# Kernel optimization log

Measured on AMD Instinct MI355X. Metric: run time of the kernel, lower is better.

The kernel has to match this reference:

```python
import jax, jax.numpy as jnp
import numpy as np

N = 65536      # samples
DX = 1024      # X features
DY = 1024      # Y features
D = 256        # projected width (x_net/y_net output)
LAMX = 0.1
LAMY = 0.1
SIGMA = 0.5    # STG gate noise std (eval-mode deterministic gate)
EPS = 0.001    # regularizer used in original code


def setup_inputs() -> dict:
    key = jax.random.key(0)
    ks = jax.random.split(key, 8)
    X = jax.random.normal(ks[0], (N, DX), dtype=jnp.float32)
    Y = jax.random.normal(ks[1], (N, DY), dtype=jnp.float32)
    # StochasticGates params (mu per input feature)
    mu_x = 0.01 * jax.random.normal(ks[2], (DX,), dtype=jnp.float32)
    mu_y = 0.01 * jax.random.normal(ks[3], (DY,), dtype=jnp.float32)
    # per-view linear nets (x_net: DX->D, y_net: DY->D)
    Wx = jax.random.normal(ks[4], (DX, D), dtype=jnp.float32) / np.sqrt(DX)
    bx = jnp.zeros((D,), dtype=jnp.float32)
    Wy = jax.random.normal(ks[5], (DY, D), dtype=jnp.float32) / np.sqrt(DY)
    by = jnp.zeros((D,), dtype=jnp.float32)
    return {"X": X, "Y": Y, "mu_x": mu_x, "mu_y": mu_y,
            "Wx": Wx, "bx": bx, "Wy": Wy, "by": by}


def _stg_gate(mu):
    # deterministic (eval) hard gate: clamp(mu + 0.5, 0, 1)
    return jnp.clip(mu + 0.5, 0.0, 1.0)


def _stg_reg(mu, lam):
    # lam * mean(P(gate > 0)) = lam * mean(Phi(mu/sigma))  [Gaussian CDF]
    return lam * jnp.mean(0.5 * (1.0 + jax.lax.erf(mu / (SIGMA * jnp.sqrt(2.0)))))


def _cov(a, b):
    # matches torch: (b.T @ a).T / (N-1) == a.T @ b / (N-1)
    n = a.shape[0]
    return (a.T @ b) / (n - 1)


def _inv_sqrt_sym(A):
    # A^(-1/2) via eigendecomposition; A symmetric so eigh == eig with V^-1 = V.T
    w, V = jnp.linalg.eigh(A)
    return (V * (w + EPS) ** (-0.5)) @ V.T


def _corr(Xh, Yh):
    d = Xh.shape[1]
    psi_x = Xh - Xh.mean(axis=0)
    psi_y = Yh - Yh.mean(axis=0)
    C_yy = _cov(psi_y, psi_y)
    C_yx = _cov(psi_y, psi_x)
    C_xy = _cov(psi_x, psi_y)
    C_xx = _cov(psi_x, psi_x)
    I = jnp.eye(d, dtype=Xh.dtype)
    C_yy_inv_root = _inv_sqrt_sym(C_yy + EPS * I)
    C_xx_inv = jnp.linalg.inv(C_xx + EPS * I)
    M = C_yy_inv_root @ C_yx @ C_xx_inv @ C_xy @ C_yy_inv_root
    return jnp.trace(M) / d


def reference(X, Y, mu_x, mu_y, Wx, bx, Wy, by):
    Xh = (X * _stg_gate(mu_x)) @ Wx + bx   # [N, D]
    Yh = (Y * _stg_gate(mu_y)) @ Wy + by   # [N, D]
    loss = -_corr(Xh, Yh) + _stg_reg(mu_x, LAMX) + _stg_reg(mu_y, LAMY)
    return loss
```

## Files before the change

kernel.cpp:

```cpp
#include <hip/hip_runtime.h>

#define N_S   65536
#define DXF   1024
#define DD    256
#define NM1   65535.0f
#define EPSR  0.001f

typedef __attribute__((ext_vector_type(4)))  float          f32x4;
typedef __attribute__((ext_vector_type(16))) float          f32x16;
typedef __attribute__((ext_vector_type(8)))  short          bf16x8;
typedef __attribute__((ext_vector_type(4)))  unsigned short ushort4_t;
typedef __attribute__((ext_vector_type(8)))  unsigned short ushort8_t;

__device__ __forceinline__ unsigned short f2bf(float f){
  unsigned u = __float_as_uint(f);
  u += 0x7fffu + ((u >> 16) & 1u);
  return (unsigned short)(u >> 16);
}
__device__ __forceinline__ float bf2f(unsigned short h){
  return __uint_as_float(((unsigned)h) << 16);
}
__device__ __forceinline__ f32x4 mfma16(bf16x8 a, bf16x8 b, f32x4 c){
  return __builtin_amdgcn_mfma_f32_16x16x32_bf16(a, b, c, 0, 0, 0);
}
__device__ __forceinline__ f32x16 mfma32(bf16x8 a, bf16x8 b, f32x16 c){
  return __builtin_amdgcn_mfma_f32_32x32x16_bf16(a, b, c, 0, 0, 0);
}
__device__ __forceinline__ void gld_lds16(const void* g, void* l){
  __builtin_amdgcn_global_load_lds(
      (const __attribute__((address_space(1))) unsigned int*)g,
      (__attribute__((address_space(3))) unsigned int*)l, 16, 0, 0);
}
__device__ __forceinline__ bf16x8 pack8(float4 a, float4 b){
  union { unsigned u[4]; bf16x8 v; } r;
  asm("v_cvt_pk_bf16_f32 %0, %1, %2" : "=v"(r.u[0]) : "v"(a.x), "v"(a.y));
  asm("v_cvt_pk_bf16_f32 %0, %1, %2" : "=v"(r.u[1]) : "v"(a.z), "v"(a.w));
  asm("v_cvt_pk_bf16_f32 %0, %1, %2" : "=v"(r.u[2]) : "v"(b.x), "v"(b.y));
  asm("v_cvt_pk_bf16_f32 %0, %1, %2" : "=v"(r.u[3]) : "v"(b.z), "v"(b.w));
  return r.v;
}

__global__ void k_prep(const float* __restrict__ Wx, const float* __restrict__ Wy,
                       const float* __restrict__ mux, const float* __restrict__ muy,
                       unsigned short* __restrict__ WTx, unsigned short* __restrict__ WTy,
                       float* __restrict__ scal){
  int v = blockIdx.y;
  const float* W  = v ? Wy  : Wx;
  const float* mu = v ? muy : mux;
  unsigned short* WT = v ? WTy : WTx;
  int j = threadIdx.x;
  if (j < 4){
    float ph = 0.5f * (1.f + erff(mu[blockIdx.x * 4 + j] * 1.41421356237f));
    atomicAdd(scal + 2 + v, 9.765625e-5f * ph);
  }
  #pragma unroll
  for (int r = 0; r < 4; ++r){
    int k = blockIdx.x * 4 + r;
    float g = fminf(fmaxf(mu[k] + 0.5f, 0.f), 1.f);
    WT[(size_t)(k >> 3) * 2048 + j * 8 + (k & 7)] = f2bf(g * W[(size_t)k * DD + j]);
  }
}

__global__ __launch_bounds__(256, 4) void k_gemm5(
    const float* __restrict__ X, const float* __restrict__ Y,
    const unsigned short* __restrict__ WTx, const unsigned short* __restrict__ WTy,
    unsigned short* __restrict__ Xhb, unsigned short* __restrict__ Yhb){
  const float* A = blockIdx.z ? Y : X;
  const unsigned short* WT = blockIdx.z ? WTy : WTx;
  unsigned short* Out = blockIdx.z ? Yhb : Xhb;

  __shared__ unsigned short As[64][40];
  __shared__ unsigned short Bs[2][4][256][8];

  int tid = threadIdx.x, lane = tid & 63, wid = tid >> 6;
  int wr = wid >> 1, wc = wid & 1;
  int row0 = blockIdx.x * 64;

  f32x4 acc[2][8] = {};

  int s_row = tid >> 2, s_kq = tid & 3;
  const float* ap = A + (size_t)(row0 + s_row) * DXF + s_kq * 8;

  auto stageB = [&](int buf, int ks){
    #pragma unroll
    for (int i = 0; i < 4; ++i)
      gld_lds16(WT + (size_t)(ks * 4 + i) * 2048 + (wid * 64 + lane) * 8,
                &Bs[buf][i][wid * 64][0]);
  };

  float4 a0, a1, n0, n1;
  stageB(0, 0);
  asm volatile("" ::: "memory");
  a0 = *(const float4*)(ap);
  a1 = *(const float4*)(ap + 4);

  for (int ks = 0; ks < 32; ++ks){
    asm volatile("s_waitcnt vmcnt(2)" ::: "memory");
    __builtin_amdgcn_s_barrier();
    if (ks + 1 < 32){
      stageB((ks + 1) & 1, ks + 1);
      asm volatile("" ::: "memory");
      n0 = *(const float4*)(ap + (ks + 1) * 32);
      n1 = *(const float4*)(ap + (ks + 1) * 32 + 4);
      asm volatile("s_waitcnt vmcnt(6)" ::: "memory");
    } else {
      asm volatile("s_waitcnt vmcnt(0)" ::: "memory");
    }
    *(bf16x8*)&As[s_row][s_kq * 8] = pack8(a0, a1);
    asm volatile("s_waitcnt lgkmcnt(0)" ::: "memory");
    __builtin_amdgcn_s_barrier();

    int bb = ks & 1;
    bf16x8 af0 = *(const bf16x8*)&As[wr * 32 + (lane & 15)][(lane >> 4) * 8];
    bf16x8 af1 = *(const bf16x8*)&As[wr * 32 + 16 + (lane & 15)][(lane >> 4) * 8];
    #pragma unroll
    for (int ni = 0; ni < 8; ++ni){
      bf16x8 bf = *(const bf16x8*)&Bs[bb][lane >> 4][wc * 128 + ni * 16 + (lane & 15)][0];
      acc[0][ni] = mfma16(af0, bf, acc[0][ni]);
      acc[1][ni] = mfma16(af1, bf, acc[1][ni]);
    }
    a0 = n0; a1 = n1;
  }

  __syncthreads();
  unsigned short* tl = &Bs[0][0][0][0];
  #pragma unroll
  for (int p = 0; p < 2; ++p){
    if (wr == p){
      #pragma unroll
      for (int mi = 0; mi < 2; ++mi)
        #pragma unroll
        for (int ni = 0; ni < 8; ++ni)
          #pragma unroll
          for (int rr = 0; rr < 4; ++rr){
            int r = mi * 16 + (lane >> 4) * 4 + rr;
            int c = wc * 128 + ni * 16 + (lane & 15);
            tl[r * 256 + c] = f2bf(acc[mi][ni][rr]);
          }
    }
    __syncthreads();
    unsigned short* ob = Out + (size_t)(row0 + p * 32) * DD;
    #pragma unroll
    for (int r = 0; r < 4; ++r){
      int off = r * 2048 + tid * 8;
      *(ushort8_t*)(ob + off) = *(const ushort8_t*)(tl + off);
    }
    if (p == 0) __syncthreads();
  }
}

__global__ __launch_bounds__(512) void k_gram(
    const unsigned short* __restrict__ Xhb, const unsigned short* __restrict__ Yhb,
    float* __restrict__ part, float* __restrict__ sx, float* __restrict__ sy, int P){
  int type = blockIdx.z;
  int p = blockIdx.x;
  int chunk = N_S / P;
  int r0 = p * chunk;
  const unsigned short* Asrc = (type == 0) ? Xhb : Yhb;
  const unsigned short* Bsrc = (type == 1) ? Yhb : Xhb;
  bool dualB = (type == 2);

  __shared__ unsigned short At[256][40];
  __shared__ unsigned short Bt[256][40];

  int tid = threadIdx.x;
  int lane = tid & 63, wid = tid >> 6;
  int wr = wid >> 1, wc = wid & 1;

  f32x4 acc[4][8] = {};
  float cs0 = 0.f, cs1 = 0.f;

  int cp  = tid & 127;
  int kb0 = tid >> 7;

  unsigned ua[2][4], ub[2][4];

  auto loadT = [&](int ks){
    int base = r0 + ks * 32;
    #pragma unroll
    for (int r = 0; r < 2; ++r){
      int kb = kb0 + r * 4;
      #pragma unroll
      for (int kr = 0; kr < 4; ++kr){
        ua[r][kr] = *(const unsigned*)(Asrc + (size_t)(base + kb * 4 + kr) * DD + cp * 2);
        if (dualB)
          ub[r][kr] = *(const unsigned*)(Bsrc + (size_t)(base + kb * 4 + kr) * DD + cp * 2);
      }
    }
  };
  auto storeT = [&](){
    #pragma unroll
    for (int r = 0; r < 2; ++r){
      int kb = kb0 + r * 4;
      ushort4_t lo = { (unsigned short)ua[r][0], (unsigned short)ua[r][1],
                       (unsigned short)ua[r][2], (unsigned short)ua[r][3] };
      ushort4_t hi = { (unsigned short)(ua[r][0] >> 16), (unsigned short)(ua[r][1] >> 16),
                       (unsigned short)(ua[r][2] >> 16), (unsigned short)(ua[r][3] >> 16) };
      *(ushort4_t*)&At[cp * 2][kb * 4]     = lo;
      *(ushort4_t*)&At[cp * 2 + 1][kb * 4] = hi;
      if (type < 2){
        #pragma unroll
        for (int kr = 0; kr < 4; ++kr){
          cs0 += bf2f((unsigned short)ua[r][kr]);
          cs1 += bf2f((unsigned short)(ua[r][kr] >> 16));
        }
      }
      if (dualB){
        ushort4_t lob = { (unsigned short)ub[r][0], (unsigned short)ub[r][1],
                          (unsigned short)ub[r][2], (unsigned short)ub[r][3] };
        ushort4_t hib = { (unsigned short)(ub[r][0] >> 16), (unsigned short)(ub[r][1] >> 16),
                          (unsigned short)(ub[r][2] >> 16), (unsigned short)(ub[r][3] >> 16) };
        *(ushort4_t*)&Bt[cp * 2][kb * 4]     = lob;
        *(ushort4_t*)&Bt[cp * 2 + 1][kb * 4] = hib;
      }
    }
  };

  unsigned short (*Btp)[40] = dualB ? Bt : At;

  int KS = chunk / 32;
  loadT(0);
  for (int ks = 0; ks < KS; ++ks){
    __syncthreads();
    storeT();
    __syncthreads();
    if (ks + 1 < KS) loadT(ks + 1);
    bf16x8 af[4], bfv[8];
    #pragma unroll
    for (int mi = 0; mi < 4; ++mi)
      af[mi] = *(const bf16x8*)&At[wr * 64 + mi * 16 + (lane & 15)][(lane >> 4) * 8];
    #pragma unroll
    for (int ni = 0; ni < 8; ++ni)
      bfv[ni] = *(const bf16x8*)&Btp[wc * 128 + ni * 16 + (lane & 15)][(lane >> 4) * 8];
    #pragma unroll
    for (int mi = 0; mi < 4; ++mi)
      #pragma unroll
      for (int ni = 0; ni < 8; ++ni)
        acc[mi][ni] = mfma16(af[mi], bfv[ni], acc[mi][ni]);
  }

  float* dst = part + ((size_t)p * 3 + type) * 65536;
  #pragma unroll
  for (int mi = 0; mi < 4; ++mi)
    #pragma unroll
    for (int ni = 0; ni < 8; ++ni)
      #pragma unroll
      for (int rr = 0; rr < 4; ++rr){
        int grow = wr * 64 + mi * 16 + (lane >> 4) * 4 + rr;
        int gcol = wc * 128 + ni * 16 + (lane & 15);
        dst[(size_t)grow * 256 + gcol] = acc[mi][ni][rr];
      }

  if (type < 2){
    __syncthreads();
    float* red = (float*)&At[0][0];
    red[kb0 * 256 + cp * 2]     = cs0;
    red[kb0 * 256 + cp * 2 + 1] = cs1;
    __syncthreads();
    if (tid < 256){
      float s = red[tid] + red[256 + tid] + red[512 + tid] + red[768 + tid];
      atomicAdd((type == 0 ? sx : sy) + tid, s);
    }
  }
}

__global__ void k_reduce(const float* __restrict__ part, const float* __restrict__ sx,
                         const float* __restrict__ sy, float* __restrict__ Am,
                         float* __restrict__ Bm,
                         unsigned short* __restrict__ Abf, unsigned short* __restrict__ Bbf,
                         unsigned short* __restrict__ Cbf, unsigned short* __restrict__ CbfT,
                         float* __restrict__ scal, int P){
  __shared__ float r2[256];
  int i = blockIdx.x, j = threadIdx.x;
  size_t idx = (size_t)i * 256 + j;
  float gxx = 0.f, gyy = 0.f, gyx = 0.f;
  for (int p = 0; p < P; ++p){
    const float* b = part + (size_t)p * 3 * 65536;
    gxx += b[idx];
    gyy += b[65536 + idx];
    gyx += b[131072 + idx];
  }
  float invn1 = 1.f / NM1;
  float invn  = 1.f / (float)N_S;
  float sxi = sx[i], sxj = sx[j], syi = sy[i], syj = sy[j];
  float diag = (i == j) ? 1.f : 0.f;
  float am = (gyy - syi * syj * invn) * invn1 + diag * (2.f * EPSR);
  float bm = (gxx - sxi * sxj * invn) * invn1 + diag * EPSR;
  float cv = (gyx - syi * sxj * invn) * invn1;
  Am[idx] = am;  Bm[idx] = bm;
  Abf[idx] = f2bf(am);
  Bbf[idx] = f2bf(bm);
  Cbf[idx] = f2bf(cv);
  CbfT[(size_t)j * 256 + i] = f2bf(cv);
  r2[j] = fabsf(am);
  __syncthreads();
  for (int s = 128; s > 0; s >>= 1){ if (j < s) r2[j] += r2[j + s]; __syncthreads(); }
  if (j == 0) atomicMax((unsigned*)scal + 5, __float_as_uint(r2[0]));
  __syncthreads();
  r2[j] = fabsf(bm);
  __syncthreads();
  for (int s = 128; s > 0; s >>= 1){ if (j < s) r2[j] += r2[j + s]; __syncthreads(); }
  if (j == 0) atomicMax((unsigned*)scal + 6, __float_as_uint(r2[0]));
}

__global__ void k_x1(const float* __restrict__ Am, const float* __restrict__ Bm,
                     unsigned short* __restrict__ X0, const float* __restrict__ scal){
  int m = blockIdx.y;
  const unsigned* su = (const unsigned*)scal;
  float al = 1.9f / __uint_as_float(su[5 + m]);
  const float* M = m ? Bm : Am;
  int e = blockIdx.x * 512 + threadIdx.x;
  float v = -al * al * M[e];
  if ((e >> 8) == (e & 255)) v += 2.f * al;
  X0[m * 65536 + e] = f2bf(v);
}

__global__ __launch_bounds__(512) void k_it(
    const unsigned short* __restrict__ Abf, const unsigned short* __restrict__ Bbf,
    const unsigned short* __restrict__ Xc, unsigned short* __restrict__ Xn){
  int m = blockIdx.y, j = blockIdx.x;
  const unsigned short* M  = m ? Bbf : Abf;
  const unsigned short* Xm = Xc + m * 65536;
  unsigned short*       Xo = Xn + m * 65536;

  __shared__ unsigned short XJ[32 * 256];
  __shared__ unsigned short TT[32 * 256];

  int tid = threadIdx.x, lane = tid & 63, w = tid >> 6;
  int r31 = lane & 31, kh = lane >> 5;

  #pragma unroll
  for (int i = 0; i < 2; ++i){
    int rl = w * 4 + i * 2 + kh;
    int cg = ((lane & 31) - rl) & 31;
    gld_lds16(Xm + (size_t)(j * 32 + rl) * 256 + cg * 8, &XJ[(w * 4 + i * 2) * 256]);
  }
  asm volatile("s_waitcnt vmcnt(0)" ::: "memory");
  __builtin_amdgcn_s_barrier();

  f32x16 acc = {};
  const unsigned short* arow = M + (size_t)(w * 32 + r31) * 256 + kh * 8;
  #pragma unroll
  for (int ks = 0; ks < 16; ++ks){
    bf16x8 af = *(const bf16x8*)(arow + ks * 16);
    int ch = ((ks * 2 + kh) + r31) & 31;
    bf16x8 bf = *(const bf16x8*)&XJ[r31 * 256 + ch * 8];
    acc = mfma32(af, bf, acc);
  }
  #pragma unroll
  for (int reg = 0; reg < 16; ++reg){
    int kk = w * 32 + (reg & 3) + ((reg >> 2) << 3) + (kh << 2);
    int ch = ((kk >> 3) + r31) & 31;
    TT[r31 * 256 + ch * 8 + (kk & 7)] = f2bf(acc[reg]);
  }
  __syncthreads();

  f32x16 acc2 = {};
  const unsigned short* xrow = Xm + (size_t)(w * 32 + r31) * 256 + kh * 8;
  #pragma unroll
  for (int ks = 0; ks < 16; ++ks){
    bf16x8 af = *(const bf16x8*)(xrow + ks * 16);
    int ch = ((ks * 2 + kh) + r31) & 31;
    bf16x8 bf = *(const bf16x8*)&TT[r31 * 256 + ch * 8];
    acc2 = mfma32(af, bf, acc2);
  }
  #pragma unroll
  for (int reg = 0; reg < 16; ++reg){
    int row = w * 32 + (reg & 3) + ((reg >> 2) << 3) + (kh << 2);
    int ch = ((row >> 3) + r31) & 31;
    float xv = bf2f(XJ[r31 * 256 + ch * 8 + (row & 7)]);
    Xo[(size_t)row * 256 + j * 32 + r31] = f2bf(2.f * xv - acc2[reg]);
  }
}

__global__ __launch_bounds__(512) void k_uv(
    const unsigned short* __restrict__ Xf,
    const unsigned short* __restrict__ Cbf, const unsigned short* __restrict__ CbfT,
    float* __restrict__ U, float* __restrict__ W){
  int m = blockIdx.y, j = blockIdx.x;
  __shared__ unsigned short BJ[32 * 256];
  int tid = threadIdx.x, lane = tid & 63, w = tid >> 6;
  int r31 = lane & 31, kh = lane >> 5;
  const unsigned short* Brows = m ? (Xf + 65536) : CbfT;
  const unsigned short* Arows = m ? Cbf : Xf;
  float* D = m ? W : U;

  #pragma unroll
  for (int i = 0; i < 2; ++i){
    int rl = w * 4 + i * 2 + kh;
    int cg = ((lane & 31) - rl) & 31;
    gld_lds16(Brows + (size_t)(j * 32 + rl) * 256 + cg * 8, &BJ[(w * 4 + i * 2) * 256]);
  }
  asm volatile("s_waitcnt vmcnt(0)" ::: "memory");
  __builtin_amdgcn_s_barrier();

  f32x16 acc = {};
  const unsigned short* ar = Arows + (size_t)(w * 32 + r31) * 256 + kh * 8;
  #pragma unroll
  for (int ks = 0; ks < 16; ++ks){
    bf16x8 af = *(const bf16x8*)(ar + ks * 16);
    int ch = ((ks * 2 + kh) + r31) & 31;
    bf16x8 bf = *(const bf16x8*)&BJ[r31 * 256 + ch * 8];
    acc = mfma32(af, bf, acc);
  }
  #pragma unroll
  for (int reg = 0; reg < 16; ++reg){
    int row = w * 32 + (reg & 3) + ((reg >> 2) << 3) + (kh << 2);
    D[(size_t)row * 256 + j * 32 + r31] = acc[reg];
  }
}

__global__ __launch_bounds__(1024) void k_fin(const float* __restrict__ U,
                                              const float* __restrict__ W,
                                              const float* __restrict__ scal,
                                              float* __restrict__ out){
  __shared__ float red[1024];
  int tid = threadIdx.x;
  float t = 0.f;
  #pragma unroll
  for (int r = 0; r < 16; ++r){
    int i = r * 4096 + tid * 4;
    float4 u = *(const float4*)(U + i);
    float4 w = *(const float4*)(W + i);
    t += u.x * w.x + u.y * w.y + u.z * w.z + u.w * w.w;
  }
  red[tid] = t; __syncthreads();
  for (int s = 512; s > 0; s >>= 1){ if (tid < s) red[tid] += red[tid + s]; __syncthreads(); }
  if (tid == 0) out[0] = -red[0] / 256.f + scal[2] + scal[3];
}

extern "C" void kernel_launch(void* const* d_in, const int* in_sizes, int n_in,
                              void* d_out, int out_size, void* d_ws, size_t ws_size,
                              hipStream_t stream){
  (void)in_sizes; (void)n_in; (void)out_size;
  const float* X   = (const float*)d_in[0];
  const float* Y   = (const float*)d_in[1];
  const float* mux = (const float*)d_in[2];
  const float* muy = (const float*)d_in[3];
  const float* Wx  = (const float*)d_in[4];
  const float* Wy  = (const float*)d_in[6];
  float* out = (float*)d_out;
  char* ws = (char*)d_ws;

  const size_t MB = 1ull << 20;
  const size_t KB = 1024;
  size_t oXHB = 0;
  size_t oYHB = 32 * MB;
  size_t oWTX = 64 * MB;
  size_t oWTY = oWTX + 512 * KB;
  size_t oSX  = oWTY + 512 * KB;
  size_t oSY  = oSX + 4 * KB;
  size_t oSC  = oSY + 4 * KB;
  size_t oA   = oSC + 4 * KB;
  size_t oB   = oA   + 256 * KB;
  size_t oABF = oB   + 256 * KB;
  size_t oBBF = oABF + 128 * KB;
  size_t oCBF = oBBF + 128 * KB;
  size_t oCBT = oCBF + 128 * KB;
  size_t oX0  = oCBT + 128 * KB;
  size_t oX1  = oX0  + 256 * KB;
  size_t oTB  = oX1  + 256 * KB;
  size_t oU   = oTB  + 256 * KB;
  size_t oV   = oU   + 256 * KB;
  size_t oPart = 68 * MB;

  size_t per = 3ull * 65536 * 4;
  int P = 128;
  while (P > 8 && oPart + (size_t)P * per > ws_size) P >>= 1;

  unsigned short* Xhb = (unsigned short*)(ws + oXHB);
  unsigned short* Yhb = (unsigned short*)(ws + oYHB);
  unsigned short* WTx = (unsigned short*)(ws + oWTX);
  unsigned short* WTy = (unsigned short*)(ws + oWTY);
  float* sx   = (float*)(ws + oSX);
  float* sy   = (float*)(ws + oSY);
  float* scal = (float*)(ws + oSC);
  float* Am   = (float*)(ws + oA);
  float* Bm   = (float*)(ws + oB);
  unsigned short* Abf  = (unsigned short*)(ws + oABF);
  unsigned short* Bbf  = (unsigned short*)(ws + oBBF);
  unsigned short* Cbf  = (unsigned short*)(ws + oCBF);
  unsigned short* CbfT = (unsigned short*)(ws + oCBT);
  unsigned short* X0   = (unsigned short*)(ws + oX0);
  unsigned short* X1   = (unsigned short*)(ws + oX1);
  float* U    = (float*)(ws + oU);
  float* V    = (float*)(ws + oV);
  float* part = (float*)(ws + oPart);

  hipMemsetAsync(ws + oSX, 0, 12 * KB, stream);

  k_prep<<<dim3(256, 2), 256, 0, stream>>>(Wx, Wy, mux, muy, WTx, WTy, scal);
  k_gemm5<<<dim3(1024, 1, 2), 256, 0, stream>>>(X, Y, WTx, WTy, Xhb, Yhb);
  k_gram<<<dim3(P, 1, 3), 512, 0, stream>>>(Xhb, Yhb, part, sx, sy, P);
  k_reduce<<<256, 256, 0, stream>>>(part, sx, sy, Am, Bm, Abf, Bbf, Cbf, CbfT, scal, P);

  k_x1<<<dim3(128, 2), 512, 0, stream>>>(Am, Bm, X0, scal);
  k_it<<<dim3(8, 2), 512, 0, stream>>>(Abf, Bbf, X0, X1);
  k_it<<<dim3(8, 2), 512, 0, stream>>>(Abf, Bbf, X1, X0);
  k_it<<<dim3(8, 2), 512, 0, stream>>>(Abf, Bbf, X0, X1);
  k_it<<<dim3(8, 2), 512, 0, stream>>>(Abf, Bbf, X1, X0);
  k_it<<<dim3(8, 2), 512, 0, stream>>>(Abf, Bbf, X0, X1);
  k_uv<<<dim3(8, 2), 512, 0, stream>>>(X1, Cbf, CbfT, U, V);
  k_fin<<<1, 1024, 0, stream>>>(U, V, scal, out);
}
```

Baseline: 345.5 us.

## Rework projection GEMM to 512 threads with single-buffered swizzled LDS B tile

```diff
diff --git a/kernel.cpp b/kernel.cpp
--- a/kernel.cpp
+++ b/kernel.cpp
@@ -30,14 +30,6 @@
   __builtin_amdgcn_global_load_lds(
       (const __attribute__((address_space(1))) unsigned int*)g,
       (__attribute__((address_space(3))) unsigned int*)l, 16, 0, 0);
-}
-__device__ __forceinline__ bf16x8 pack8(float4 a, float4 b){
-  union { unsigned u[4]; bf16x8 v; } r;
-  asm("v_cvt_pk_bf16_f32 %0, %1, %2" : "=v"(r.u[0]) : "v"(a.x), "v"(a.y));
-  asm("v_cvt_pk_bf16_f32 %0, %1, %2" : "=v"(r.u[1]) : "v"(a.z), "v"(a.w));
-  asm("v_cvt_pk_bf16_f32 %0, %1, %2" : "=v"(r.u[2]) : "v"(b.x), "v"(b.y));
-  asm("v_cvt_pk_bf16_f32 %0, %1, %2" : "=v"(r.u[3]) : "v"(b.z), "v"(b.w));
-  return r.v;
 }
 
 __global__ void k_prep(const float* __restrict__ Wx, const float* __restrict__ Wy,
@@ -61,7 +53,7 @@
   }
 }
 
-__global__ __launch_bounds__(256, 4) void k_gemm5(
+__global__ __launch_bounds__(512, 8) void k_gemm7(
     const float* __restrict__ X, const float* __restrict__ Y,
     const unsigned short* __restrict__ WTx, const unsigned short* __restrict__ WTy,
     unsigned short* __restrict__ Xhb, unsigned short* __restrict__ Yhb){
@@ -70,79 +62,87 @@
   unsigned short* Out = blockIdx.z ? Yhb : Xhb;
 
   __shared__ unsigned short As[64][40];
-  __shared__ unsigned short Bs[2][4][256][8];
+  __shared__ unsigned short Bs[4][256][8];
 
   int tid = threadIdx.x, lane = tid & 63, wid = tid >> 6;
   int wr = wid >> 1, wc = wid & 1;
   int row0 = blockIdx.x * 64;
 
-  f32x4 acc[2][8] = {};
-
-  int s_row = tid >> 2, s_kq = tid & 3;
-  const float* ap = A + (size_t)(row0 + s_row) * DXF + s_kq * 8;
-
-  auto stageB = [&](int buf, int ks){
-    #pragma unroll
-    for (int i = 0; i < 4; ++i)
-      gld_lds16(WT + (size_t)(ks * 4 + i) * 2048 + (wid * 64 + lane) * 8,
-                &Bs[buf][i][wid * 64][0]);
+  f32x4 acc[8] = {};
+
+  int s_row = tid >> 3, s_kq = tid & 7;
+  const float* ap = A + (size_t)(row0 + s_row) * DXF + s_kq * 4;
+
+  auto stageB = [&](int ks){
+    #pragma unroll
+    for (int i = 0; i < 2; ++i){
+      int cl = ((wid >> 2) * 2 + i) * 64 + lane;
+      int csw = cl ^ ((cl >> 1) & 4);
+      gld_lds16(WT + (size_t)(ks * 4 + (wid & 3)) * 2048 + csw * 8,
+                &Bs[wid & 3][((wid >> 2) * 2 + i) * 64][0]);
+    }
   };
-
-  float4 a0, a1, n0, n1;
-  stageB(0, 0);
+  auto storeAs = [&](float4 a){
+    union { unsigned u[2]; ushort4_t v; } r;
+    asm("v_cvt_pk_bf16_f32 %0, %1, %2" : "=v"(r.u[0]) : "v"(a.x), "v"(a.y));
+    asm("v_cvt_pk_bf16_f32 %0, %1, %2" : "=v"(r.u[1]) : "v"(a.z), "v"(a.w));
+    *(ushort4_t*)&As[s_row][s_kq * 4] = r.v;
+  };
+
+  const unsigned short* bb = &Bs[0][0][0] + (lane >> 4) * 2048 + wc * 1024
+                           + (((lane & 15) * 8) ^ ((lane & 8) << 2));
+
+  float4 a0;
+  stageB(0);
   asm volatile("" ::: "memory");
   a0 = *(const float4*)(ap);
-  a1 = *(const float4*)(ap + 4);
+  asm volatile("s_waitcnt vmcnt(0)" ::: "memory");
+  storeAs(a0);
+  a0 = *(const float4*)(ap + 32);
+  asm volatile("s_waitcnt lgkmcnt(0)" ::: "memory");
+  __builtin_amdgcn_s_barrier();
 
   for (int ks = 0; ks < 32; ++ks){
+    bf16x8 af = *(const bf16x8*)&As[wr * 16 + (lane & 15)][(lane >> 4) * 8];
+    #pragma unroll
+    for (int ni = 0; ni < 8; ++ni){
+      bf16x8 bf = *(const bf16x8*)(bb + ni * 128);
+      acc[ni] = mfma16(af, bf, acc[ni]);
+    }
+    if (ks == 31) break;
+    __builtin_amdgcn_s_barrier();
+    stageB(ks + 1);
     asm volatile("s_waitcnt vmcnt(2)" ::: "memory");
-    __builtin_amdgcn_s_barrier();
-    if (ks + 1 < 32){
-      stageB((ks + 1) & 1, ks + 1);
-      asm volatile("" ::: "memory");
-      n0 = *(const float4*)(ap + (ks + 1) * 32);
-      n1 = *(const float4*)(ap + (ks + 1) * 32 + 4);
-      asm volatile("s_waitcnt vmcnt(6)" ::: "memory");
+    storeAs(a0);
+    if (ks + 2 < 32){
+      a0 = *(const float4*)(ap + (ks + 2) * 32);
+      asm volatile("s_waitcnt vmcnt(1)" ::: "memory");
     } else {
       asm volatile("s_waitcnt vmcnt(0)" ::: "memory");
     }
-    *(bf16x8*)&As[s_row][s_kq * 8] = pack8(a0, a1);
     asm volatile("s_waitcnt lgkmcnt(0)" ::: "memory");
     __builtin_amdgcn_s_barrier();
-
-    int bb = ks & 1;
-    bf16x8 af0 = *(const bf16x8*)&As[wr * 32 + (lane & 15)][(lane >> 4) * 8];
-    bf16x8 af1 = *(const bf16x8*)&As[wr * 32 + 16 + (lane & 15)][(lane >> 4) * 8];
-    #pragma unroll
-    for (int ni = 0; ni < 8; ++ni){
-      bf16x8 bf = *(const bf16x8*)&Bs[bb][lane >> 4][wc * 128 + ni * 16 + (lane & 15)][0];
-      acc[0][ni] = mfma16(af0, bf, acc[0][ni]);
-      acc[1][ni] = mfma16(af1, bf, acc[1][ni]);
-    }
-    a0 = n0; a1 = n1;
   }
 
   __syncthreads();
-  unsigned short* tl = &Bs[0][0][0][0];
+  unsigned short* tl = &Bs[0][0][0];
   #pragma unroll
   for (int p = 0; p < 2; ++p){
-    if (wr == p){
+    if ((wr >> 1) == p){
       #pragma unroll
-      for (int mi = 0; mi < 2; ++mi)
+      for (int ni = 0; ni < 8; ++ni)
         #pragma unroll
-        for (int ni = 0; ni < 8; ++ni)
-          #pragma unroll
-          for (int rr = 0; rr < 4; ++rr){
-            int r = mi * 16 + (lane >> 4) * 4 + rr;
-            int c = wc * 128 + ni * 16 + (lane & 15);
-            tl[r * 256 + c] = f2bf(acc[mi][ni][rr]);
-          }
+        for (int rr = 0; rr < 4; ++rr){
+          int r = (wr & 1) * 16 + (lane >> 4) * 4 + rr;
+          int c = wc * 128 + ni * 16 + (lane & 15);
+          tl[r * 256 + c] = f2bf(acc[ni][rr]);
+        }
     }
     __syncthreads();
     unsigned short* ob = Out + (size_t)(row0 + p * 32) * DD;
     #pragma unroll
-    for (int r = 0; r < 4; ++r){
-      int off = r * 2048 + tid * 8;
+    for (int r = 0; r < 2; ++r){
+      int off = r * 4096 + tid * 8;
       *(ushort8_t*)(ob + off) = *(const ushort8_t*)(tl + off);
     }
     if (p == 0) __syncthreads();
@@ -465,7 +465,7 @@
   size_t oPart = 68 * MB;
 
   size_t per = 3ull * 65536 * 4;
-  int P = 128;
+  int P = 64;
   while (P > 8 && oPart + (size_t)P * per > ws_size) P >>= 1;
 
   unsigned short* Xhb = (unsigned short*)(ws + oXHB);
@@ -490,7 +490,7 @@
   hipMemsetAsync(ws + oSX, 0, 12 * KB, stream);
 
   k_prep<<<dim3(256, 2), 256, 0, stream>>>(Wx, Wy, mux, muy, WTx, WTy, scal);
-  k_gemm5<<<dim3(1024, 1, 2), 256, 0, stream>>>(X, Y, WTx, WTy, Xhb, Yhb);
+  k_gemm7<<<dim3(1024, 1, 2), 512, 0, stream>>>(X, Y, WTx, WTy, Xhb, Yhb);
   k_gram<<<dim3(P, 1, 3), 512, 0, stream>>>(Xhb, Yhb, part, sx, sy, P);
   k_reduce<<<256, 256, 0, stream>>>(part, sx, sy, Am, Bm, Abf, Bbf, Cbf, CbfT, scal, P);
 
```

After: 318.3 us. 7.8% less time.
